# Kernel optimization log

Measured on AMD Instinct MI355X. Metric: run time of the kernel, lower is better.

Reference implementation:

```python
import jax, jax.numpy as jnp
import numpy as np

BSZ, T, ENC, HID = 128, 512, 128, 128


def setup_inputs() -> dict:
    key = jax.random.key(0)
    ks = jax.random.split(key, 8)
    encoder_output = jax.random.normal(ks[0], (BSZ, T, ENC), dtype=jnp.float32)
    lengths = jax.random.randint(ks[1], (BSZ,), 4, T + 1)
    mask = (jnp.arange(T)[None, :] < lengths[:, None]).astype(jnp.int32)
    s = 1.0 / np.sqrt(HID)  # torch LSTM init range
    W_ih = jax.random.uniform(ks[2], (4 * HID, ENC), jnp.float32, -s, s)
    W_hh = jax.random.uniform(ks[3], (4 * HID, HID), jnp.float32, -s, s)
    b_ih = jax.random.uniform(ks[4], (4 * HID,), jnp.float32, -s, s)
    b_hh = jax.random.uniform(ks[5], (4 * HID,), jnp.float32, -s, s)
    s2 = 1.0 / np.sqrt(HID + ENC)  # torch Linear init range
    fc_w = jax.random.uniform(ks[6], (1, HID + ENC), jnp.float32, -s2, s2)
    fc_b = jax.random.uniform(ks[7], (1,), jnp.float32, -s2, s2)
    return {"encoder_output": encoder_output, "mask": mask, "W_ih": W_ih,
            "W_hh": W_hh, "b_ih": b_ih, "b_hh": b_hh, "fc_w": fc_w, "fc_b": fc_b}


def _lstm_last(src, W_ih, W_hh, b_ih, b_hh):
    # src: [N, 3, E] -> last hidden state [N, H]; torch gate order i,f,g,o
    N = src.shape[0]
    H = W_hh.shape[1]
    h0 = jnp.zeros((N, H), src.dtype)
    c0 = jnp.zeros((N, H), src.dtype)

    def step(carry, x):
        h, c = carry
        gates = x @ W_ih.T + h @ W_hh.T + b_ih + b_hh
        i, f, g, o = jnp.split(gates, 4, axis=-1)
        c = jax.nn.sigmoid(f) * c + jax.nn.sigmoid(i) * jnp.tanh(g)
        h = jax.nn.sigmoid(o) * jnp.tanh(c)
        return (h, c), None

    (h, _), _ = jax.lax.scan(step, (h0, c0), jnp.swapaxes(src, 0, 1))
    return h


def reference(encoder_output, mask, W_ih, W_hh, b_ih, b_hh, fc_w, fc_b):
    B, Tn, E = encoder_output.shape
    H = W_hh.shape[1]
    lengths = jnp.sum(mask, axis=1)                       # [B]
    J = Tn - 3                                            # number of window starts
    # his_turn_states: encoder_output zeroed beyond each length
    states = encoder_output * mask[..., None].astype(encoder_output.dtype)
    # sliding windows of 3 consecutive turn states: [B, J, 3, E]
    src = jnp.stack([states[:, 0:J], states[:, 1:J + 1], states[:, 2:J + 2]], axis=2)
    h_last = _lstm_last(src.reshape(B * J, 3, E), W_ih, W_hh, b_ih, b_hh)
    h_last = h_last.reshape(B, J, H)                      # [B, J, H]
    # con_fc(concat(h, tgt)) decomposes: w_h.h + w_e.tgt + b
    w = fc_w[0]
    a = h_last @ w[:H]                                    # [B, J]
    cterm = states @ w[H:]                                # [B, T]
    logits = a[:, :, None] + cterm[:, None, :] + fc_b[0]  # [B, J, T]
    j_idx = jnp.arange(J)
    k_idx = jnp.arange(Tn)
    valid_k = (k_idx[None, None, :] >= (j_idx[None, :, None] + 3)) & \
              (k_idx[None, None, :] < lengths[:, None, None])    # candidate mask
    valid_pair = (j_idx[None, :] <= (lengths[:, None] - 4))       # [B, J]
    neg = jnp.asarray(-1e9, logits.dtype)
    lse = jax.nn.logsumexp(jnp.where(valid_k, logits, neg), axis=-1)  # [B, J]
    pos_idx = jnp.broadcast_to((j_idx + 3)[None, :, None], (B, J, 1))
    pos = jnp.take_along_axis(logits, pos_idx, axis=2)[..., 0]        # [B, J]
    loss_pair = lse - pos                                 # CE with target index 0
    vp = valid_pair.astype(logits.dtype)
    dli_loss = jnp.sum(loss_pair * vp) / jnp.sum(vp)
    return dli_loss
```

## Files before the change

kernel.cpp:

```cpp
#include <hip/hip_runtime.h>
#include <math.h>

#define BSZ 128
#define T   512
#define E   128
#define H   128


__global__ __launch_bounds__(256) void dli_dot_kernel(
    const float* __restrict__ enc,
    const int*   __restrict__ mask,
    const float* __restrict__ fc_w,
    float*       __restrict__ cterm,
    double*      __restrict__ accum,
    int*         __restrict__ scan_done)
{
    const int t = threadIdx.x;
    if (blockIdx.x == 0 && t == 0) {
        accum[0] = 0.0;
        accum[1] = 0.0;
        *scan_done = 0;
    }
    const int wid  = t >> 6;
    const int lane = t & 63;
    const int sub  = lane >> 5;
    const int li   = lane & 31;
    const long row = (long)blockIdx.x * 8 + wid * 2 + sub;

    if ((row & (T - 1)) < 3) return;
    if (mask[row] == 0) return;

    const float4 w4 = *reinterpret_cast<const float4*>(fc_w + H + 4 * li);
    const float4 v  = *reinterpret_cast<const float4*>(enc + row * E + 4 * li);
    float p = v.x * w4.x + v.y * w4.y + v.z * w4.z + v.w * w4.w;
    #pragma unroll
    for (int off = 16; off >= 1; off >>= 1)
        p += __shfl_xor(p, off);
    if (li == 0) cterm[row] = p;
}

__global__ __launch_bounds__(T) void dli_scan_kernel(
    const float* __restrict__ cterm,
    const int*   __restrict__ mask,
    double*      __restrict__ accum,
    int*         __restrict__ scan_done,
    float*       __restrict__ out)
{
    const int b    = blockIdx.x;
    const int t    = threadIdx.x;
    const int lane = t & 63;
    const int wid  = t >> 6;

    __shared__ float s_c[T];
    __shared__ float s_red[8];
    __shared__ int   s_lw[8];
    __shared__ float s_M;

    const int mv = mask[b * T + t];
    unsigned long long bal = __ballot(mv != 0);
    if (lane == 0) s_lw[wid] = __popcll(bal);
    s_c[t] = mv ? cterm[b * T + t] : 0.0f;
    __syncthreads();

    int len = 0;
    #pragma unroll
    for (int i = 0; i < 8; ++i) len += s_lw[i];

    const bool act = (t >= 3 && t < len);

    float mval = act ? s_c[t] : -INFINITY;
    #pragma unroll
    for (int off = 32; off >= 1; off >>= 1)
        mval = fmaxf(mval, __shfl_xor(mval, off));
    if (lane == 0) s_red[wid] = mval;
    __syncthreads();
    if (t == 0) {
        float m = s_red[0];
        #pragma unroll
        for (int i = 1; i < 8; ++i) m = fmaxf(m, s_red[i]);
        s_M = m;
    }
    __syncthreads();
    const float Mrow = s_M;

    float x = act ? expf(s_c[t] - Mrow) : 0.0f;
    #pragma unroll
    for (int off = 1; off < 64; off <<= 1) {
        float y = __shfl_down(x, off);
        if (lane + off < 64) x += y;
    }
    if (lane == 0) s_red[wid] = x;
    __syncthreads();
    float tail = 0.0f;
    for (int w = wid + 1; w < 8; ++w) tail += s_red[w];
    float term = act ? (Mrow + logf(x + tail) - s_c[t]) : 0.0f;
    __syncthreads();

    #pragma unroll
    for (int off = 32; off >= 1; off >>= 1)
        term += __shfl_xor(term, off);
    if (lane == 0) s_red[wid] = term;
    __syncthreads();

    if (t == 0) {
        float rs = 0.0f;
        #pragma unroll
        for (int i = 0; i < 8; ++i) rs += s_red[i];
        int cnt = len - 3; if (cnt < 0) cnt = 0;
        atomicAdd(&accum[0], (double)rs);
        atomicAdd(&accum[1], (double)cnt);
        __threadfence();
        int old = atomicAdd(scan_done, 1);
        if (old == BSZ - 1) {
            __threadfence();
            double a0 = atomicAdd(&accum[0], 0.0);
            double a1 = atomicAdd(&accum[1], 0.0);
            out[0] = (float)(a0 / a1);
        }
    }
}

extern "C" void kernel_launch(void* const* d_in, const int* in_sizes, int n_in,
                              void* d_out, int out_size, void* d_ws, size_t ws_size,
                              hipStream_t stream) {
    const float* enc  = (const float*)d_in[0];
    const int*   mask = (const int*)d_in[1];
    const float* fc_w = (const float*)d_in[6];

    double* accum     = (double*)d_ws;
    int*    scan_done = (int*)((char*)d_ws + 16);
    float*  cterm     = (float*)((char*)d_ws + 1024);

    dli_dot_kernel<<<(BSZ * T) / 8, 256, 0, stream>>>(enc, mask, fc_w, cterm,
                                                      accum, scan_done);
    dli_scan_kernel<<<BSZ, T, 0, stream>>>(cterm, mask, accum, scan_done,
                                           (float*)d_out);
}
```

Before: 96.00 us.

## Fuse dot-product and scan kernels into one per-batch 1024-thread kernel

```diff
diff --git a/kernel.cpp b/kernel.cpp
--- a/kernel.cpp
+++ b/kernel.cpp
@@ -7,41 +7,10 @@
 #define H   128
 
 
-__global__ __launch_bounds__(256) void dli_dot_kernel(
+__global__ __launch_bounds__(1024) void dli_fused_kernel(
     const float* __restrict__ enc,
     const int*   __restrict__ mask,
     const float* __restrict__ fc_w,
-    float*       __restrict__ cterm,
-    double*      __restrict__ accum,
-    int*         __restrict__ scan_done)
-{
-    const int t = threadIdx.x;
-    if (blockIdx.x == 0 && t == 0) {
-        accum[0] = 0.0;
-        accum[1] = 0.0;
-        *scan_done = 0;
-    }
-    const int wid  = t >> 6;
-    const int lane = t & 63;
-    const int sub  = lane >> 5;
-    const int li   = lane & 31;
-    const long row = (long)blockIdx.x * 8 + wid * 2 + sub;
-
-    if ((row & (T - 1)) < 3) return;
-    if (mask[row] == 0) return;
-
-    const float4 w4 = *reinterpret_cast<const float4*>(fc_w + H + 4 * li);
-    const float4 v  = *reinterpret_cast<const float4*>(enc + row * E + 4 * li);
-    float p = v.x * w4.x + v.y * w4.y + v.z * w4.z + v.w * w4.w;
-    #pragma unroll
-    for (int off = 16; off >= 1; off >>= 1)
-        p += __shfl_xor(p, off);
-    if (li == 0) cterm[row] = p;
-}
-
-__global__ __launch_bounds__(T) void dli_scan_kernel(
-    const float* __restrict__ cterm,
-    const int*   __restrict__ mask,
     double*      __restrict__ accum,
     int*         __restrict__ scan_done,
     float*       __restrict__ out)
@@ -50,29 +19,49 @@
     const int t    = threadIdx.x;
     const int lane = t & 63;
     const int wid  = t >> 6;
+    const int hw   = t >> 5;
+    const int li   = t & 31;
 
     __shared__ float s_c[T];
     __shared__ float s_red[8];
     __shared__ int   s_lw[8];
     __shared__ float s_M;
 
-    const int mv = mask[b * T + t];
-    unsigned long long bal = __ballot(mv != 0);
-    if (lane == 0) s_lw[wid] = __popcll(bal);
-    s_c[t] = mv ? cterm[b * T + t] : 0.0f;
+    if (t < T) {
+        const int mv = mask[b * T + t];
+        unsigned long long bal = __ballot(mv != 0);
+        if (lane == 0) s_lw[wid] = __popcll(bal);
+    }
     __syncthreads();
-
     int len = 0;
     #pragma unroll
     for (int i = 0; i < 8; ++i) len += s_lw[i];
 
-    const bool act = (t >= 3 && t < len);
+    const float4 w4 = *reinterpret_cast<const float4*>(fc_w + H + 4 * li);
+    const float* erow = enc + (long)b * T * E;
+    #pragma unroll 4
+    for (int r0 = 3; r0 < len; r0 += 32) {
+        int r_raw = r0 + hw;
+        int r = r_raw < len ? r_raw : len - 1;
+        const float4 v = *reinterpret_cast<const float4*>(erow + (long)r * E + 4 * li);
+        float p = v.x * w4.x + v.y * w4.y + v.z * w4.z + v.w * w4.w;
+        #pragma unroll
+        for (int off = 16; off >= 1; off >>= 1)
+            p += __shfl_xor(p, off);
+        if (li == 0 && r_raw < len) s_c[r_raw] = p;
+    }
+    __syncthreads();
+
+    const bool sth = (t < T);
+    const bool act = sth && (t >= 3 && t < len);
 
     float mval = act ? s_c[t] : -INFINITY;
-    #pragma unroll
-    for (int off = 32; off >= 1; off >>= 1)
-        mval = fmaxf(mval, __shfl_xor(mval, off));
-    if (lane == 0) s_red[wid] = mval;
+    if (sth) {
+        #pragma unroll
+        for (int off = 32; off >= 1; off >>= 1)
+            mval = fmaxf(mval, __shfl_xor(mval, off));
+        if (lane == 0) s_red[wid] = mval;
+    }
     __syncthreads();
     if (t == 0) {
         float m = s_red[0];
@@ -84,29 +73,36 @@
     const float Mrow = s_M;
 
     float x = act ? expf(s_c[t] - Mrow) : 0.0f;
-    #pragma unroll
-    for (int off = 1; off < 64; off <<= 1) {
-        float y = __shfl_down(x, off);
-        if (lane + off < 64) x += y;
+    if (sth) {
+        #pragma unroll
+        for (int off = 1; off < 64; off <<= 1) {
+            float y = __shfl_down(x, off);
+            if (lane + off < 64) x += y;
+        }
+        if (lane == 0) s_red[wid] = x;
     }
-    if (lane == 0) s_red[wid] = x;
     __syncthreads();
-    float tail = 0.0f;
-    for (int w = wid + 1; w < 8; ++w) tail += s_red[w];
-    float term = act ? (Mrow + logf(x + tail) - s_c[t]) : 0.0f;
+    float term = 0.0f;
+    if (act) {
+        float tail = 0.0f;
+        for (int w = wid + 1; w < 8; ++w) tail += s_red[w];
+        term = Mrow + logf(x + tail) - s_c[t];
+    }
     __syncthreads();
 
-    #pragma unroll
-    for (int off = 32; off >= 1; off >>= 1)
-        term += __shfl_xor(term, off);
-    if (lane == 0) s_red[wid] = term;
+    if (sth) {
+        #pragma unroll
+        for (int off = 32; off >= 1; off >>= 1)
+            term += __shfl_xor(term, off);
+        if (lane == 0) s_red[wid] = term;
+    }
     __syncthreads();
 
     if (t == 0) {
         float rs = 0.0f;
         #pragma unroll
         for (int i = 0; i < 8; ++i) rs += s_red[i];
-        int cnt = len - 3; if (cnt < 0) cnt = 0;
+        int cnt = len - 3;
         atomicAdd(&accum[0], (double)rs);
         atomicAdd(&accum[1], (double)cnt);
         __threadfence();
@@ -129,10 +125,9 @@
 
     double* accum     = (double*)d_ws;
     int*    scan_done = (int*)((char*)d_ws + 16);
-    float*  cterm     = (float*)((char*)d_ws + 1024);
 
-    dli_dot_kernel<<<(BSZ * T) / 8, 256, 0, stream>>>(enc, mask, fc_w, cterm,
-                                                      accum, scan_done);
-    dli_scan_kernel<<<BSZ, T, 0, stream>>>(cterm, mask, accum, scan_done,
-                                           (float*)d_out);
+    hipMemsetAsync(d_ws, 0, 32, stream);
+
+    dli_fused_kernel<<<BSZ, 1024, 0, stream>>>(enc, mask, fc_w, accum, scan_done,
+                                               (float*)d_out);
 }
```

Measured after the change: 94.29 us. No clear change (-1.8%).
